# Kernel optimization log

Measured on AMD Instinct MI355X. Metric: run time of the kernel, lower is better.

## Reference

```python
import jax, jax.numpy as jnp
import numpy as np

N6 = 524288          # nodes at depth 6 (full-octree batch of 2)
N5 = N6 // 8         # 65536 nodes at depth 5
N4 = N5 // 8         # 8192 nodes at depth 4
EPS = 1e-5           # torch BatchNorm1d default eps


def _pool(x):
    # octree_max_pool on a full octree: 8 contiguous children -> parent max
    n, c = x.shape
    return jnp.max(x.reshape(n // 8, 8, c), axis=1)


def _up(x):
    # octree_upsample on a full octree: each parent broadcast to its 8 children
    return jnp.repeat(x, 8, axis=0)


def _conv1x1_bn_relu(x, w, g, b):
    # Conv1x1 (Linear, no bias) + BatchNorm1d (training-mode batch stats) + ReLU
    y = x @ w                              # [N, Cout]
    m = jnp.mean(y, axis=0)
    v = jnp.var(y, axis=0)                 # biased variance, as in torch BN
    y = (y - m) * jax.lax.rsqrt(v + EPS) * g + b
    return jax.nn.relu(y)


def setup_inputs() -> dict:
    key = jax.random.key(0)
    ks = jax.random.split(key, 8)
    s = 0.02
    return {
        "data0": jax.random.normal(ks[0], (N6, 96), jnp.float32),
        "data1": jax.random.normal(ks[1], (N5, 192), jnp.float32),
        "w01": jax.random.normal(ks[2], (96, 192), jnp.float32) * s,
        "g01": jnp.ones((192,), jnp.float32),
        "b01": jnp.zeros((192,), jnp.float32),
        "w02": jax.random.normal(ks[3], (96, 384), jnp.float32) * s,
        "g02": jnp.ones((384,), jnp.float32),
        "b02": jnp.zeros((384,), jnp.float32),
        "w10": jax.random.normal(ks[4], (192, 96), jnp.float32) * s,
        "g10": jnp.ones((96,), jnp.float32),
        "b10": jnp.zeros((96,), jnp.float32),
        "w12": jax.random.normal(ks[5], (192, 384), jnp.float32) * s,
        "g12": jnp.ones((384,), jnp.float32),
        "b12": jnp.zeros((384,), jnp.float32),
        "depth": 6,
    }


def reference(data0, data1, w01, g01, b01, w02, g02, b02,
              w10, g10, b10, w12, g12, b12, depth):
    # channels = [96, 192, 384]; data0 at depth, data1 at depth-1.
    # out[j] = sum_i TransFunc(channels[i]->channels[j])(data[i], depth-i -> depth-j)
    # j=0 (depth, 96ch):   identity(data0) + upsample(conv10(data1))
    out0 = data0 + _up(_conv1x1_bn_relu(data1, w10, g10, b10))
    # j=1 (depth-1, 192ch): conv01(pool(data0)) + identity(data1)
    p0 = _pool(data0)                      # [N5, 96]
    out1 = _conv1x1_bn_relu(p0, w01, g01, b01) + data1
    # j=2 (depth-2, 384ch): conv02(pool^2(data0)) + conv12(pool(data1))
    out2 = (_conv1x1_bn_relu(_pool(p0), w02, g02, b02)
            + _conv1x1_bn_relu(_pool(data1), w12, g12, b12))
    return (out0, out1, out2)
```

## Files before the change

kernel.cpp:

```cpp
#include <hip/hip_runtime.h>

typedef unsigned short u16;
typedef __attribute__((ext_vector_type(8))) short short8;
typedef __attribute__((ext_vector_type(4))) float f4;
typedef __attribute__((ext_vector_type(4))) unsigned short u16x4;

#define CN6 524288
#define CN5 65536
#define CN4 8192

__device__ inline u16 f2bf(float f){
  unsigned u = __float_as_uint(f);
  return (u16)((u + 0x7FFFu + ((u >> 16) & 1u)) >> 16);
}
__device__ inline float bf2f(u16 h){ return __uint_as_float(((unsigned)h) << 16); }

__device__ inline f4 nt_load4(const float* p){
  return __builtin_nontemporal_load(reinterpret_cast<const f4*>(p));
}
__device__ inline void nt_store4(float* p, f4 v){
  __builtin_nontemporal_store(v, reinterpret_cast<f4*>(p));
}


__global__ __launch_bounds__(256) void k_prep(const float* __restrict__ w10, const float* __restrict__ w01,
                                              const float* __restrict__ w02, const float* __restrict__ w12,
                                              u16* __restrict__ wT10, u16* __restrict__ wT01,
                                              u16* __restrict__ wT02, u16* __restrict__ wT12,
                                              float* __restrict__ stats){
  int i = blockIdx.x * 256 + threadIdx.x;
  if (i < 2112) stats[i] = 0.f;
  if (i < 18432){ int j = i / 192, k = i - j * 192; wT10[i] = f2bf(w10[k * 96 + j]); }
  else if (i < 36864){ int e = i - 18432; int j = e / 96, k = e - j * 96; wT01[e] = f2bf(w01[k * 192 + j]); }
  else if (i < 73728){ int e = i - 36864; int j = e / 96, k = e - j * 96; wT02[e] = f2bf(w02[k * 384 + j]); }
  else if (i < 147456){ int e = i - 73728; int j = e / 192, k = e - j * 192; wT12[e] = f2bf(w12[k * 384 + j]); }
}

__global__ __launch_bounds__(256) void k_gemm10p(const float* __restrict__ d1, const u16* __restrict__ wT10,
                                                 u16* __restrict__ y10, u16* __restrict__ p1,
                                                 float* __restrict__ stats){
  __shared__ u16 sm[64 * 200];
  __shared__ float ls[96], lq[96];
  int tid = threadIdx.x, bid = blockIdx.x;
  if (tid < 96){ ls[tid] = 0.f; lq[tid] = 0.f; }

  if (tid < 192){
    int p = tid / 24, c8 = tid - p * 24;
    f4 v0[8], v1[8];
    #pragma unroll
    for (int r = 0; r < 8; r++){
      const float* src = d1 + ((size_t)bid * 64 + p * 8 + r) * 192 + c8 * 8;
      v0[r] = *reinterpret_cast<const f4*>(src);
      v1[r] = *reinterpret_cast<const f4*>(src + 4);
    }
    float mx[8];
    #pragma unroll
    for (int q = 0; q < 4; q++){ mx[q] = v0[0][q]; mx[4 + q] = v1[0][q]; }
    #pragma unroll
    for (int r = 0; r < 8; r++){
      short8 h;
      #pragma unroll
      for (int q = 0; q < 4; q++){
        h[q]     = (short)f2bf(v0[r][q]);
        h[4 + q] = (short)f2bf(v1[r][q]);
        if (r){ mx[q] = fmaxf(mx[q], v0[r][q]); mx[4 + q] = fmaxf(mx[4 + q], v1[r][q]); }
      }
      *reinterpret_cast<short8*>(&sm[(p * 8 + r) * 200 + c8 * 8]) = h;
    }
    short8 hp;
    #pragma unroll
    for (int q = 0; q < 8; q++) hp[q] = (short)f2bf(mx[q]);
    *reinterpret_cast<short8*>(p1 + ((size_t)bid * 8 + p) * 192 + c8 * 8) = hp;
  }
  __syncthreads();

  int lane = tid & 63, wave = tid >> 6;
  int arowl = wave * 16 + (lane & 15);
  int k0 = (lane >> 4) * 8;
  short8 af[6];
  #pragma unroll
  for (int s = 0; s < 6; s++) af[s] = *reinterpret_cast<short8*>(&sm[arowl * 200 + s * 32 + k0]);

  int colb = lane & 15, rgrp = (lane >> 4) * 4;
  int row0 = bid * 64 + wave * 16;
  #pragma unroll
  for (int j = 0; j < 6; j++){
    int col = j * 16 + colb;
    f4 acc = {0.f, 0.f, 0.f, 0.f};
    const u16* wr = wT10 + (size_t)col * 192 + k0;
    #pragma unroll
    for (int s = 0; s < 6; s++)
      acc = __builtin_amdgcn_mfma_f32_16x16x32_bf16(af[s], *reinterpret_cast<const short8*>(wr + s * 32), acc, 0, 0, 0);
    float s1 = 0.f, s2 = 0.f;
    #pragma unroll
    for (int r = 0; r < 4; r++){
      y10[(size_t)(row0 + rgrp + r) * 96 + col] = f2bf(acc[r]);
      s1 += acc[r]; s2 += acc[r] * acc[r];
    }
    atomicAdd(&ls[col], s1);
    atomicAdd(&lq[col], s2);
  }
  __syncthreads();
  if (tid < 96){ atomicAdd(&stats[tid], ls[tid]); atomicAdd(&stats[1056 + tid], lq[tid]); }
}

__global__ __launch_bounds__(192) void k_out0(const float* __restrict__ d0, const u16* __restrict__ y10,
                                              const float* __restrict__ stats,
                                              const float* __restrict__ g10, const float* __restrict__ b10,
                                              float* __restrict__ out0, u16* __restrict__ p0, u16* __restrict__ p00){
  __shared__ float aL[96], cL[96];
  __shared__ float sp[8][96];
  int tid = threadIdx.x, gp = blockIdx.x;
  if (tid < 96){
    float m = stats[tid] * (1.f / 65536.f);
    float v = stats[1056 + tid] * (1.f / 65536.f) - m * m;
    float a = g10[tid] * rsqrtf(v + 1e-5f);
    aL[tid] = a; cL[tid] = b10[tid] - m * a;
  }
  __syncthreads();

  int p = tid / 24, c4 = tid - p * 24;
  int par = gp * 8 + p;
  u16x4 yb = *reinterpret_cast<const u16x4*>(y10 + (size_t)par * 96 + c4 * 4);
  size_t base = ((size_t)par * 8) * 96 + c4 * 4;

  f4 v[8];
  #pragma unroll
  for (int r = 0; r < 8; r++) v[r] = nt_load4(d0 + base + r * 96);

  f4 yv;
  #pragma unroll
  for (int q = 0; q < 4; q++){
    int c = c4 * 4 + q;
    yv[q] = fmaxf(bf2f((u16)yb[q]) * aL[c] + cL[c], 0.f);
  }
  f4 mx = v[0];
  #pragma unroll
  for (int r = 1; r < 8; r++)
    #pragma unroll
    for (int q = 0; q < 4; q++) mx[q] = fmaxf(mx[q], v[r][q]);

  #pragma unroll
  for (int r = 0; r < 8; r++){
    f4 o;
    #pragma unroll
    for (int q = 0; q < 4; q++) o[q] = v[r][q] + yv[q];
    nt_store4(out0 + base + r * 96, o);
  }

  u16x4 hp;
  #pragma unroll
  for (int q = 0; q < 4; q++) hp[q] = f2bf(mx[q]);
  *reinterpret_cast<u16x4*>(p0 + (size_t)par * 96 + c4 * 4) = hp;
  *reinterpret_cast<f4*>(&sp[p][c4 * 4]) = mx;
  __syncthreads();

  if (tid < 24){
    f4 m = *reinterpret_cast<f4*>(&sp[0][tid * 4]);
    #pragma unroll
    for (int pp = 1; pp < 8; pp++){
      f4 x = *reinterpret_cast<f4*>(&sp[pp][tid * 4]);
      #pragma unroll
      for (int q = 0; q < 4; q++) m[q] = fmaxf(m[q], x[q]);
    }
    u16x4 h;
    #pragma unroll
    for (int q = 0; q < 4; q++) h[q] = f2bf(m[q]);
    *reinterpret_cast<u16x4*>(p00 + (size_t)gp * 96 + tid * 4) = h;
  }
}

template<int Ci, int Co>
__device__ __forceinline__ void stats_body(const u16* __restrict__ x, const u16* __restrict__ wT,
                                           float* __restrict__ sum, float* __restrict__ sq,
                                           int bid, float* ls, float* lq){
  int tid = threadIdx.x;
  for (int t = tid; t < Co; t += 256){ ls[t] = 0.f; lq[t] = 0.f; }
  __syncthreads();
  int lane = tid & 63, wave = tid >> 6;
  int arow = bid * 64 + wave * 16 + (lane & 15);
  int k0 = (lane >> 4) * 8;
  constexpr int KS = Ci / 32;
  short8 af[KS];
  const u16* xr = x + (size_t)arow * Ci + k0;
  #pragma unroll
  for (int s = 0; s < KS; s++) af[s] = *reinterpret_cast<const short8*>(xr + s * 32);
  int colb = lane & 15;
  #pragma unroll 4
  for (int j = 0; j < Co / 16; j++){
    int col = j * 16 + colb;
    f4 acc = {0.f, 0.f, 0.f, 0.f};
    const u16* wr = wT + (size_t)col * Ci + k0;
    #pragma unroll
    for (int s = 0; s < KS; s++)
      acc = __builtin_amdgcn_mfma_f32_16x16x32_bf16(af[s], *reinterpret_cast<const short8*>(wr + s * 32), acc, 0, 0, 0);
    float s1 = acc[0] + acc[1] + acc[2] + acc[3];
    float s2 = acc[0]*acc[0] + acc[1]*acc[1] + acc[2]*acc[2] + acc[3]*acc[3];
    atomicAdd(&ls[col], s1);
    atomicAdd(&lq[col], s2);
  }
  __syncthreads();
  for (int t = tid; t < Co; t += 256){ atomicAdd(&sum[t], ls[t]); atomicAdd(&sq[t], lq[t]); }
}

__global__ __launch_bounds__(256) void k_statsAll(const u16* __restrict__ p0, const u16* __restrict__ p00,
                                                  const u16* __restrict__ p1,
                                                  const u16* __restrict__ wT01, const u16* __restrict__ wT02,
                                                  const u16* __restrict__ wT12, float* __restrict__ stats){
  __shared__ float ls[384], lq[384];
  int bid = blockIdx.x;
  if (bid < 1024)      stats_body<96, 192>(p0,  wT01, stats + 96,  stats + 1056 + 96,  bid,        ls, lq);
  else if (bid < 1152) stats_body<96, 384>(p00, wT02, stats + 288, stats + 1056 + 288, bid - 1024, ls, lq);
  else                 stats_body<192,384>(p1,  wT12, stats + 672, stats + 1056 + 672, bid - 1152, ls, lq);
}

__global__ __launch_bounds__(256) void k_out1(const u16* __restrict__ p0, const u16* __restrict__ wT01,
                                              const float* __restrict__ d1, const float* __restrict__ stats,
                                              const float* __restrict__ g01, const float* __restrict__ b01,
                                              float* __restrict__ out1){
  __shared__ float aL[192], cL[192];
  int tid = threadIdx.x, bid = blockIdx.x;
  if (tid < 192){
    float m = stats[96 + tid] * (1.f / 65536.f);
    float v = stats[1056 + 96 + tid] * (1.f / 65536.f) - m * m;
    float a = g01[tid] * rsqrtf(v + 1e-5f);
    aL[tid] = a; cL[tid] = b01[tid] - m * a;
  }
  __syncthreads();
  int lane = tid & 63, wave = tid >> 6;
  int row0 = bid * 64 + wave * 16;
  int arow = row0 + (lane & 15);
  int k0 = (lane >> 4) * 8;
  short8 af[3];
  const u16* xr = p0 + (size_t)arow * 96 + k0;
  #pragma unroll
  for (int s = 0; s < 3; s++) af[s] = *reinterpret_cast<const short8*>(xr + s * 32);
  int colb = lane & 15, rgrp = (lane >> 4) * 4;
  #pragma unroll 4
  for (int j = 0; j < 12; j++){
    int col = j * 16 + colb;
    f4 acc = {0.f, 0.f, 0.f, 0.f};
    const u16* wr = wT01 + (size_t)col * 96 + k0;
    #pragma unroll
    for (int s = 0; s < 3; s++)
      acc = __builtin_amdgcn_mfma_f32_16x16x32_bf16(af[s], *reinterpret_cast<const short8*>(wr + s * 32), acc, 0, 0, 0);
    float a = aL[col], c = cL[col];
    #pragma unroll
    for (int r = 0; r < 4; r++){
      size_t off = (size_t)(row0 + rgrp + r) * 192 + col;
      float dv = __builtin_nontemporal_load(d1 + off);
      __builtin_nontemporal_store(fmaxf(acc[r] * a + c, 0.f) + dv, out1 + off);
    }
  }
}

__global__ __launch_bounds__(256) void k_out2(const u16* __restrict__ p00, const u16* __restrict__ p1,
                                              const u16* __restrict__ wT02, const u16* __restrict__ wT12,
                                              const float* __restrict__ stats,
                                              const float* __restrict__ g02, const float* __restrict__ b02,
                                              const float* __restrict__ g12, const float* __restrict__ b12,
                                              float* __restrict__ out2){
  __shared__ float a2[384], c2[384], a1[384], c1[384];
  int tid = threadIdx.x, bid = blockIdx.x;
  for (int t = tid; t < 384; t += 256){
    float m = stats[288 + t] * (1.f / 8192.f);
    float v = stats[1056 + 288 + t] * (1.f / 8192.f) - m * m;
    float a = g02[t] * rsqrtf(v + 1e-5f);
    a2[t] = a; c2[t] = b02[t] - m * a;
    m = stats[672 + t] * (1.f / 8192.f);
    v = stats[1056 + 672 + t] * (1.f / 8192.f) - m * m;
    a = g12[t] * rsqrtf(v + 1e-5f);
    a1[t] = a; c1[t] = b12[t] - m * a;
  }
  __syncthreads();
  int lane = tid & 63, wave = tid >> 6;
  int row0 = bid * 64 + wave * 16;
  int arow = row0 + (lane & 15);
  int k0 = (lane >> 4) * 8;
  short8 aA[3], aB[6];
  const u16* x0 = p00 + (size_t)arow * 96 + k0;
  #pragma unroll
  for (int s = 0; s < 3; s++) aA[s] = *reinterpret_cast<const short8*>(x0 + s * 32);
  const u16* x1 = p1 + (size_t)arow * 192 + k0;
  #pragma unroll
  for (int s = 0; s < 6; s++) aB[s] = *reinterpret_cast<const short8*>(x1 + s * 32);
  int colb = lane & 15, rgrp = (lane >> 4) * 4;
  #pragma unroll 2
  for (int j = 0; j < 24; j++){
    int col = j * 16 + colb;
    f4 u = {0.f, 0.f, 0.f, 0.f}, w = {0.f, 0.f, 0.f, 0.f};
    const u16* wr2 = wT02 + (size_t)col * 96 + k0;
    #pragma unroll
    for (int s = 0; s < 3; s++)
      u = __builtin_amdgcn_mfma_f32_16x16x32_bf16(aA[s], *reinterpret_cast<const short8*>(wr2 + s * 32), u, 0, 0, 0);
    const u16* wr1 = wT12 + (size_t)col * 192 + k0;
    #pragma unroll
    for (int s = 0; s < 6; s++)
      w = __builtin_amdgcn_mfma_f32_16x16x32_bf16(aB[s], *reinterpret_cast<const short8*>(wr1 + s * 32), w, 0, 0, 0);
    #pragma unroll
    for (int r = 0; r < 4; r++){
      float o = fmaxf(u[r] * a2[col] + c2[col], 0.f) + fmaxf(w[r] * a1[col] + c1[col], 0.f);
      __builtin_nontemporal_store(o, out2 + (size_t)(row0 + rgrp + r) * 384 + col);
    }
  }
}

extern "C" void kernel_launch(void* const* d_in, const int* in_sizes, int n_in,
                              void* d_out, int out_size, void* d_ws, size_t ws_size,
                              hipStream_t stream){
  const float* data0 = (const float*)d_in[0];
  const float* data1 = (const float*)d_in[1];
  const float* w01 = (const float*)d_in[2];
  const float* g01 = (const float*)d_in[3];
  const float* b01 = (const float*)d_in[4];
  const float* w02 = (const float*)d_in[5];
  const float* g02 = (const float*)d_in[6];
  const float* b02 = (const float*)d_in[7];
  const float* w10 = (const float*)d_in[8];
  const float* g10 = (const float*)d_in[9];
  const float* b10 = (const float*)d_in[10];
  const float* w12 = (const float*)d_in[11];
  const float* g12 = (const float*)d_in[12];
  const float* b12 = (const float*)d_in[13];

  float* out0 = (float*)d_out;
  float* out1 = out0 + (size_t)CN6 * 96;
  float* out2 = out1 + (size_t)CN5 * 192;

  char* ws = (char*)d_ws;
  u16* p1   = (u16*)(ws + 0);
  u16* p0   = (u16*)(ws + 3145728);
  u16* p00  = (u16*)(ws + 15728640);
  u16* y10  = (u16*)(ws + 17301504);
  u16* wT10 = (u16*)(ws + 29884416);
  u16* wT01 = (u16*)(ws + 29921280);
  u16* wT02 = (u16*)(ws + 29958144);
  u16* wT12 = (u16*)(ws + 30031872);
  float* stats = (float*)(ws + 30179328);

  k_prep<<<576, 256, 0, stream>>>(w10, w01, w02, w12, wT10, wT01, wT02, wT12, stats);
  k_gemm10p<<<1024, 256, 0, stream>>>(data1, wT10, y10, p1, stats);
  k_out0<<<8192, 192, 0, stream>>>(data0, y10, stats, g10, b10, out0, p0, p00);
  k_statsAll<<<1280, 256, 0, stream>>>(p0, p00, p1, wT01, wT02, wT12, stats);
  k_out1<<<1024, 256, 0, stream>>>(p0, wT01, data1, stats, g01, b01, out1);
  k_out2<<<128, 256, 0, stream>>>(p00, p1, wT02, wT12, stats, g02, b02, g12, b12, out2);
}
```

Before: 239.6 us.

## Transpose MFMA operands for row-contiguous stores and stage outputs through LDS

The MFMA operand order is swapped so each lane owns one row and four consecutive channels. This lets y10 be written as 4-wide bf16 vectors, and lets out1 and out2 tiles be staged in shared memory and then written with coalesced 16-byte nontemporal stores. The BN statistics for conv10 move out of the GEMM into a separate k_stats10 kernel that re-reads y10, which costs an extra launch and an extra pass over y10. k_out2 is split across twice as many blocks, each covering half the rows with two waves per row group, to raise parallelism.

```diff
diff --git a/kernel.cpp b/kernel.cpp
--- a/kernel.cpp
+++ b/kernel.cpp
@@ -37,12 +37,9 @@
 }
 
 __global__ __launch_bounds__(256) void k_gemm10p(const float* __restrict__ d1, const u16* __restrict__ wT10,
-                                                 u16* __restrict__ y10, u16* __restrict__ p1,
-                                                 float* __restrict__ stats){
+                                                 u16* __restrict__ y10, u16* __restrict__ p1){
   __shared__ u16 sm[64 * 200];
-  __shared__ float ls[96], lq[96];
   int tid = threadIdx.x, bid = blockIdx.x;
-  if (tid < 96){ ls[tid] = 0.f; lq[tid] = 0.f; }
 
   if (tid < 192){
     int p = tid / 24, c8 = tid - p * 24;
@@ -75,30 +72,50 @@
   __syncthreads();
 
   int lane = tid & 63, wave = tid >> 6;
-  int arowl = wave * 16 + (lane & 15);
-  int k0 = (lane >> 4) * 8;
-  short8 af[6];
-  #pragma unroll
-  for (int s = 0; s < 6; s++) af[s] = *reinterpret_cast<short8*>(&sm[arowl * 200 + s * 32 + k0]);
-
-  int colb = lane & 15, rgrp = (lane >> 4) * 4;
-  int row0 = bid * 64 + wave * 16;
+  int colb = lane & 15;
+  int k0 = (lane >> 4) * 8, rgrp = (lane >> 4) * 4;
+  int arowl = wave * 16 + colb;
+  short8 xf[6];
+  #pragma unroll
+  for (int s = 0; s < 6; s++) xf[s] = *reinterpret_cast<short8*>(&sm[arowl * 200 + s * 32 + k0]);
+
+  size_t xrow = (size_t)bid * 64 + arowl;
   #pragma unroll
   for (int j = 0; j < 6; j++){
-    int col = j * 16 + colb;
     f4 acc = {0.f, 0.f, 0.f, 0.f};
-    const u16* wr = wT10 + (size_t)col * 192 + k0;
+    const u16* wr = wT10 + (size_t)(j * 16 + colb) * 192 + k0;
     #pragma unroll
     for (int s = 0; s < 6; s++)
-      acc = __builtin_amdgcn_mfma_f32_16x16x32_bf16(af[s], *reinterpret_cast<const short8*>(wr + s * 32), acc, 0, 0, 0);
-    float s1 = 0.f, s2 = 0.f;
-    #pragma unroll
-    for (int r = 0; r < 4; r++){
-      y10[(size_t)(row0 + rgrp + r) * 96 + col] = f2bf(acc[r]);
-      s1 += acc[r]; s2 += acc[r] * acc[r];
-    }
-    atomicAdd(&ls[col], s1);
-    atomicAdd(&lq[col], s2);
+      acc = __builtin_amdgcn_mfma_f32_16x16x32_bf16(*reinterpret_cast<const short8*>(wr + s * 32), xf[s], acc, 0, 0, 0);
+    u16x4 h;
+    #pragma unroll
+    for (int r = 0; r < 4; r++) h[r] = f2bf(acc[r]);
+    *reinterpret_cast<u16x4*>(y10 + xrow * 96 + j * 16 + rgrp) = h;
+  }
+}
+
+__global__ __launch_bounds__(192) void k_stats10(const u16* __restrict__ y10, float* __restrict__ stats){
+  __shared__ float ls[96], lq[96];
+  int tid = threadIdx.x, bid = blockIdx.x;
+  if (tid < 96){ ls[tid] = 0.f; lq[tid] = 0.f; }
+  __syncthreads();
+  int c8 = tid % 12, rl = tid / 12;
+  float s1[8], s2[8];
+  #pragma unroll
+  for (int q = 0; q < 8; q++){ s1[q] = 0.f; s2[q] = 0.f; }
+  for (int it = 0; it < 32; it++){
+    size_t row = (size_t)bid * 512 + it * 16 + rl;
+    short8 h = *reinterpret_cast<const short8*>(y10 + row * 96 + c8 * 8);
+    #pragma unroll
+    for (int q = 0; q < 8; q++){
+      float v = bf2f((u16)h[q]);
+      s1[q] += v; s2[q] += v * v;
+    }
+  }
+  #pragma unroll
+  for (int q = 0; q < 8; q++){
+    atomicAdd(&ls[c8 * 8 + q], s1[q]);
+    atomicAdd(&lq[c8 * 8 + q], s2[q]);
   }
   __syncthreads();
   if (tid < 96){ atomicAdd(&stats[tid], ls[tid]); atomicAdd(&stats[1056 + tid], lq[tid]); }
@@ -219,6 +236,7 @@
                                               const float* __restrict__ g01, const float* __restrict__ b01,
                                               float* __restrict__ out1){
   __shared__ float aL[192], cL[192];
+  __shared__ float so[64 * 196];
   int tid = threadIdx.x, bid = blockIdx.x;
   if (tid < 192){
     float m = stats[96 + tid] * (1.f / 65536.f);
@@ -228,29 +246,43 @@
   }
   __syncthreads();
   int lane = tid & 63, wave = tid >> 6;
-  int row0 = bid * 64 + wave * 16;
-  int arow = row0 + (lane & 15);
-  int k0 = (lane >> 4) * 8;
-  short8 af[3];
-  const u16* xr = p0 + (size_t)arow * 96 + k0;
-  #pragma unroll
-  for (int s = 0; s < 3; s++) af[s] = *reinterpret_cast<const short8*>(xr + s * 32);
-  int colb = lane & 15, rgrp = (lane >> 4) * 4;
+  int colb = lane & 15;
+  int k0 = (lane >> 4) * 8, rgrp = (lane >> 4) * 4;
+  int rowl = wave * 16 + colb;
+  short8 xf[3];
+  const u16* xr = p0 + ((size_t)bid * 64 + rowl) * 96 + k0;
+  #pragma unroll
+  for (int s = 0; s < 3; s++) xf[s] = *reinterpret_cast<const short8*>(xr + s * 32);
   #pragma unroll 4
   for (int j = 0; j < 12; j++){
-    int col = j * 16 + colb;
+    int ch0 = j * 16 + rgrp;
     f4 acc = {0.f, 0.f, 0.f, 0.f};
-    const u16* wr = wT01 + (size_t)col * 96 + k0;
+    const u16* wr = wT01 + (size_t)(j * 16 + colb) * 96 + k0;
     #pragma unroll
     for (int s = 0; s < 3; s++)
-      acc = __builtin_amdgcn_mfma_f32_16x16x32_bf16(af[s], *reinterpret_cast<const short8*>(wr + s * 32), acc, 0, 0, 0);
-    float a = aL[col], c = cL[col];
+      acc = __builtin_amdgcn_mfma_f32_16x16x32_bf16(*reinterpret_cast<const short8*>(wr + s * 32), xf[s], acc, 0, 0, 0);
+    f4 o;
     #pragma unroll
     for (int r = 0; r < 4; r++){
-      size_t off = (size_t)(row0 + rgrp + r) * 192 + col;
-      float dv = __builtin_nontemporal_load(d1 + off);
-      __builtin_nontemporal_store(fmaxf(acc[r] * a + c, 0.f) + dv, out1 + off);
-    }
+      int ch = ch0 + r;
+      o[r] = fmaxf(acc[r] * aL[ch] + cL[ch], 0.f);
+    }
+    *reinterpret_cast<f4*>(&so[rowl * 196 + ch0]) = o;
+  }
+  __syncthreads();
+  const float* d1b = d1 + (size_t)bid * 64 * 192;
+  float* o1b = out1 + (size_t)bid * 64 * 192;
+  #pragma unroll
+  for (int i = 0; i < 12; i++){
+    int idx = i * 256 + tid;
+    int rl = idx / 48, c4 = idx % 48;
+    f4 y = *reinterpret_cast<f4*>(&so[rl * 196 + c4 * 4]);
+    int off = rl * 192 + c4 * 4;
+    f4 g = nt_load4(d1b + off);
+    f4 o;
+    #pragma unroll
+    for (int q = 0; q < 4; q++) o[q] = y[q] + g[q];
+    nt_store4(o1b + off, o);
   }
 }
 
@@ -261,6 +293,7 @@
                                               const float* __restrict__ g12, const float* __restrict__ b12,
                                               float* __restrict__ out2){
   __shared__ float a2[384], c2[384], a1[384], c1[384];
+  __shared__ float so[32 * 392];
   int tid = threadIdx.x, bid = blockIdx.x;
   for (int t = tid; t < 384; t += 256){
     float m = stats[288 + t] * (1.f / 8192.f);
@@ -274,34 +307,44 @@
   }
   __syncthreads();
   int lane = tid & 63, wave = tid >> 6;
-  int row0 = bid * 64 + wave * 16;
-  int arow = row0 + (lane & 15);
-  int k0 = (lane >> 4) * 8;
-  short8 aA[3], aB[6];
-  const u16* x0 = p00 + (size_t)arow * 96 + k0;
-  #pragma unroll
-  for (int s = 0; s < 3; s++) aA[s] = *reinterpret_cast<const short8*>(x0 + s * 32);
-  const u16* x1 = p1 + (size_t)arow * 192 + k0;
-  #pragma unroll
-  for (int s = 0; s < 6; s++) aB[s] = *reinterpret_cast<const short8*>(x1 + s * 32);
-  int colb = lane & 15, rgrp = (lane >> 4) * 4;
+  int wr2 = wave >> 1, wc = wave & 1;
+  int colb = lane & 15;
+  int k0 = (lane >> 4) * 8, rgrp = (lane >> 4) * 4;
+  int rowl = wr2 * 16 + colb;
+  size_t arow = (size_t)bid * 32 + rowl;
+  short8 xA[3], xB[6];
+  #pragma unroll
+  for (int s = 0; s < 3; s++) xA[s] = *reinterpret_cast<const short8*>(p00 + arow * 96 + k0 + s * 32);
+  #pragma unroll
+  for (int s = 0; s < 6; s++) xB[s] = *reinterpret_cast<const short8*>(p1 + arow * 192 + k0 + s * 32);
   #pragma unroll 2
-  for (int j = 0; j < 24; j++){
-    int col = j * 16 + colb;
+  for (int j = 0; j < 12; j++){
+    int ch0 = wc * 192 + j * 16 + rgrp;
+    int wrow = wc * 192 + j * 16 + colb;
     f4 u = {0.f, 0.f, 0.f, 0.f}, w = {0.f, 0.f, 0.f, 0.f};
-    const u16* wr2 = wT02 + (size_t)col * 96 + k0;
+    const u16* wra = wT02 + (size_t)wrow * 96 + k0;
     #pragma unroll
     for (int s = 0; s < 3; s++)
-      u = __builtin_amdgcn_mfma_f32_16x16x32_bf16(aA[s], *reinterpret_cast<const short8*>(wr2 + s * 32), u, 0, 0, 0);
-    const u16* wr1 = wT12 + (size_t)col * 192 + k0;
+      u = __builtin_amdgcn_mfma_f32_16x16x32_bf16(*reinterpret_cast<const short8*>(wra + s * 32), xA[s], u, 0, 0, 0);
+    const u16* wrb = wT12 + (size_t)wrow * 192 + k0;
     #pragma unroll
     for (int s = 0; s < 6; s++)
-      w = __builtin_amdgcn_mfma_f32_16x16x32_bf16(aB[s], *reinterpret_cast<const short8*>(wr1 + s * 32), w, 0, 0, 0);
+      w = __builtin_amdgcn_mfma_f32_16x16x32_bf16(*reinterpret_cast<const short8*>(wrb + s * 32), xB[s], w, 0, 0, 0);
+    f4 o;
     #pragma unroll
     for (int r = 0; r < 4; r++){
-      float o = fmaxf(u[r] * a2[col] + c2[col], 0.f) + fmaxf(w[r] * a1[col] + c1[col], 0.f);
-      __builtin_nontemporal_store(o, out2 + (size_t)(row0 + rgrp + r) * 384 + col);
-    }
+      int ch = ch0 + r;
+      o[r] = fmaxf(u[r] * a2[ch] + c2[ch], 0.f) + fmaxf(w[r] * a1[ch] + c1[ch], 0.f);
+    }
+    *reinterpret_cast<f4*>(&so[rowl * 392 + ch0]) = o;
+  }
+  __syncthreads();
+  #pragma unroll
+  for (int i = 0; i < 12; i++){
+    int idx = i * 256 + tid;
+    int rl = idx / 96, c4 = idx % 96;
+    f4 v = *reinterpret_cast<f4*>(&so[rl * 392 + c4 * 4]);
+    nt_store4(out2 + ((size_t)bid * 32 + rl) * 384 + c4 * 4, v);
   }
 }
 
@@ -339,9 +382,10 @@
   float* stats = (float*)(ws + 30179328);
 
   k_prep<<<576, 256, 0, stream>>>(w10, w01, w02, w12, wT10, wT01, wT02, wT12, stats);
-  k_gemm10p<<<1024, 256, 0, stream>>>(data1, wT10, y10, p1, stats);
+  k_gemm10p<<<1024, 256, 0, stream>>>(data1, wT10, y10, p1);
+  k_stats10<<<128, 192, 0, stream>>>(y10, stats);
   k_out0<<<8192, 192, 0, stream>>>(data0, y10, stats, g10, b10, out0, p0, p00);
   k_statsAll<<<1280, 256, 0, stream>>>(p0, p00, p1, wT01, wT02, wT12, stats);
   k_out1<<<1024, 256, 0, stream>>>(p0, wT01, data1, stats, g01, b01, out1);
-  k_out2<<<128, 256, 0, stream>>>(p00, p1, wT02, wT12, stats, g02, b02, g12, b12, out2);
-}
+  k_out2<<<256, 256, 0, stream>>>(p00, p1, wT02, wT12, stats, g02, b02, g12, b12, out2);
+}
```

Measured after the change: 215.0 us. 10.3% less time.
